# Kernel optimization log

Measured on AMD Instinct MI355X. Metric: run time of the kernel, lower is better.

## Reference

```python
import jax, jax.numpy as jnp
import numpy as np

EMBED = 768
HEADS = 12
HEAD_DIM = EMBED // HEADS
HIDDEN = int(EMBED * 4.0)
EPS = 1e-5


def setup_inputs() -> dict:
    key = jax.random.key(0)
    ks = jax.random.split(key, 12)
    s = 0.02
    return {
        "x": jax.random.normal(ks[0], (8, 1024, EMBED), dtype=jnp.float32),
        # norm1 / norm2 (LayerNorm affine params)
        "g1": jnp.ones((EMBED,), jnp.float32),
        "b1": jnp.zeros((EMBED,), jnp.float32),
        "g2": jnp.ones((EMBED,), jnp.float32),
        "b2": jnp.zeros((EMBED,), jnp.float32),
        # attention weights (stored [in, out]; qkv_bias=False)
        "w_qkv": jax.random.normal(ks[1], (EMBED, 3 * EMBED), jnp.float32) * s,
        "w_proj": jax.random.normal(ks[2], (EMBED, EMBED), jnp.float32) * s,
        "b_proj": jnp.zeros((EMBED,), jnp.float32),
        # MLP weights
        "w_fc1": jax.random.normal(ks[3], (EMBED, HIDDEN), jnp.float32) * s,
        "b_fc1": jnp.zeros((HIDDEN,), jnp.float32),
        "w_fc2": jax.random.normal(ks[4], (HIDDEN, EMBED), jnp.float32) * s,
        "b_fc2": jnp.zeros((EMBED,), jnp.float32),
    }


def _layernorm(x, g, b):
    mu = jnp.mean(x, axis=-1, keepdims=True)
    var = jnp.var(x, axis=-1, keepdims=True)
    return (x - mu) * jax.lax.rsqrt(var + EPS) * g + b


def reference(x, g1, b1, g2, b2, w_qkv, w_proj, b_proj, w_fc1, b_fc1, w_fc2, b_fc2):
    B, N, C = x.shape
    scaling = HEAD_DIM ** (-0.5)

    # --- attention branch ---
    h = _layernorm(x, g1, b1)
    qkv = (h @ w_qkv).reshape(B, N, 3, HEADS, HEAD_DIM)
    q, k, v = qkv[:, :, 0], qkv[:, :, 1], qkv[:, :, 2]  # [B, N, H, D]
    attn = jnp.einsum("bnhd,bmhd->bhnm", q, k) * scaling  # full NxN scores
    attn = jax.nn.softmax(attn, axis=-1)
    out = jnp.einsum("bhnm,bmhd->bnhd", attn, v).reshape(B, N, C)
    out = out @ w_proj + b_proj
    x = x + out

    # --- MLP branch ---
    h = _layernorm(x, g2, b2)
    h = jax.nn.gelu(h @ w_fc1 + b_fc1, approximate=False)
    h = h @ w_fc2 + b_fc2
    return x + h
```

## Files before the change

### kernel.cpp

```cpp
#include <hip/hip_runtime.h>
#include <hip/hip_bf16.h>
#include <math.h>

#define EMBED 768
#define HEADS 12
#define HEAD_DIM 64
#define HIDDEN 3072
#define SEQ 1024
#define BATCH 8
#define TOKENS (SEQ*BATCH)

typedef unsigned short u16;
typedef __attribute__((ext_vector_type(8))) short bf16x8;
typedef __attribute__((ext_vector_type(4))) float floatx4;
typedef __attribute__((ext_vector_type(4))) u16 u16x4;
typedef __attribute__((ext_vector_type(2))) u16 u16x2;

__device__ __forceinline__ u16 f2bf(float f){
    union { float f; unsigned u; } v; v.f = f;
    unsigned r = v.u + 0x7fffu + ((v.u >> 16) & 1u);
    return (u16)(r >> 16);
}

__device__ __forceinline__ void gload16(const void* g, void* l){
    __builtin_amdgcn_global_load_lds((const __attribute__((address_space(1))) void*)g,
                                     (__attribute__((address_space(3))) void*)l, 16, 0, 0);
}

__device__ __forceinline__ float gelu_fast(float x){
    float t = 1.5957691216f * (x + 0.044715f * x * x * x);
    return x / (1.0f + __expf(-t));
}

__global__ void transpose_cast_all(const float* __restrict__ w0, const float* __restrict__ w1,
                                   const float* __restrict__ w2, const float* __restrict__ w3,
                                   u16* __restrict__ o0, u16* __restrict__ o1,
                                   u16* __restrict__ o2, u16* __restrict__ o3){
    int bb = blockIdx.x;
    const float* W; u16* Wt; int K, N, bx, by;
    if(bb < 1728)      { int l = bb;        W=w0; Wt=o0; K=768;  N=2304; bx=l%72; by=l/72; }
    else if(bb < 2304) { int l = bb-1728;   W=w1; Wt=o1; K=768;  N=768;  bx=l%24; by=l/24; }
    else if(bb < 4608) { int l = bb-2304;   W=w2; Wt=o2; K=768;  N=3072; bx=l%96; by=l/96; }
    else               { int l = bb-4608;   W=w3; Wt=o3; K=3072; N=768;  bx=l%24; by=l/24; }

    __shared__ float tile[32][33];
    int n0 = bx * 32, k0 = by * 32;
    int tx = threadIdx.x, ty = threadIdx.y;
    #pragma unroll
    for(int i=0;i<32;i+=8) tile[ty+i][tx] = W[(size_t)(k0+ty+i)*N + n0+tx];
    __syncthreads();
    int tid = ty*32 + tx;
    int kp = (tid & 15)*2, nn = tid >> 4;
    #pragma unroll
    for(int p=0;p<2;p++){
        int n = nn + p*16;
        u16x2 w2v;
        w2v.x = f2bf(tile[kp  ][n]);
        w2v.y = f2bf(tile[kp+1][n]);
        *(u16x2*)(Wt + (size_t)(n0+n)*K + k0 + kp) = w2v;
    }
}

__global__ __launch_bounds__(256) void ln_kernel(const float* __restrict__ x, const float* __restrict__ g,
                                                 const float* __restrict__ b, u16* __restrict__ out){
    int row  = blockIdx.x * 4 + (threadIdx.x >> 6);
    int lane = threadIdx.x & 63;
    const float4* xr = (const float4*)(x + (size_t)row * EMBED);
    float4 v[3];
    float s = 0.f;
    #pragma unroll
    for(int i=0;i<3;i++){
        v[i] = xr[i*64 + lane];
        s += v[i].x + v[i].y + v[i].z + v[i].w;
    }
    #pragma unroll
    for(int o=32;o>0;o>>=1) s += __shfl_xor(s, o);
    float mu = s * (1.0f/EMBED);
    float s2 = 0.f;
    #pragma unroll
    for(int i=0;i<3;i++){
        float dx = v[i].x-mu, dy = v[i].y-mu, dz = v[i].z-mu, dw = v[i].w-mu;
        s2 += dx*dx + dy*dy + dz*dz + dw*dw;
    }
    #pragma unroll
    for(int o=32;o>0;o>>=1) s2 += __shfl_xor(s2, o);
    float rstd = rsqrtf(s2*(1.0f/EMBED) + 1e-5f);
    u16* orow = out + (size_t)row * EMBED;
    const float4* g4 = (const float4*)g;
    const float4* b4 = (const float4*)b;
    #pragma unroll
    for(int i=0;i<3;i++){
        int c4 = i*64 + lane;
        float4 gv = g4[c4], bv = b4[c4];
        u16x4 pk;
        pk.x = f2bf((v[i].x-mu)*rstd*gv.x + bv.x);
        pk.y = f2bf((v[i].y-mu)*rstd*gv.y + bv.y);
        pk.z = f2bf((v[i].z-mu)*rstd*gv.z + bv.z);
        pk.w = f2bf((v[i].w-mu)*rstd*gv.w + bv.w);
        *(u16x4*)(orow + c4*4) = pk;
    }
}

template<int EPI, int BM>
__global__ __launch_bounds__(256) void gemm_bt(const u16* __restrict__ A, const u16* __restrict__ Bt,
        void* __restrict__ Cout, const float* __restrict__ bias, const float* __restrict__ res,
        u16* __restrict__ vt, int M, int N, int K, int ldc){
    constexpr int MF  = BM/32;
    constexpr int ASZ = BM*64;
    constexpr int BSZ = 128*64;
    __shared__ __align__(16) u16 As[2*ASZ];
    __shared__ __align__(16) u16 Bs[2*BSZ];
    int tid  = threadIdx.x;
    int wave = tid >> 6, lane = tid & 63;
    int quad = lane >> 4, lm = lane & 15;
    int m0 = blockIdx.y * BM, n0 = blockIdx.x * 128;
    int wm = (wave & 1) * (BM/2);
    int wn = (wave >> 1) * 64;

    floatx4 acc[MF][4];
    #pragma unroll
    for(int i=0;i<MF;i++)
        #pragma unroll
        for(int j=0;j<4;j++) acc[i][j] = (floatx4){0.f,0.f,0.f,0.f};

    int srow = tid >> 3;
    int scol = ((tid & 7) ^ (srow & 7)) * 8;
    const u16* aP[MF];
    const u16* bP[4];
    #pragma unroll
    for(int p=0;p<MF;p++) aP[p] = A  + (size_t)(m0 + p*32 + srow) * K + scol;
    #pragma unroll
    for(int p=0;p<4;p++)  bP[p] = Bt + (size_t)(n0 + p*32 + srow) * K + scol;

    #pragma unroll
    for(int p=0;p<MF;p++) gload16(aP[p], As + p*2048 + tid*8);
    #pragma unroll
    for(int p=0;p<4;p++)  gload16(bP[p], Bs + p*2048 + tid*8);
    __syncthreads();

    int cur = 0;
    for(int k0=0; k0<K; k0+=64){
        int nxt = cur ^ 1;
        if(k0 + 64 < K){
            #pragma unroll
            for(int p=0;p<MF;p++) gload16(aP[p] + k0 + 64, As + nxt*ASZ + p*2048 + tid*8);
            #pragma unroll
            for(int p=0;p<4;p++)  gload16(bP[p] + k0 + 64, Bs + nxt*BSZ + p*2048 + tid*8);
        }
        const u16* Asb = As + cur*ASZ;
        const u16* Bsb = Bs + cur*BSZ;
        #pragma unroll
        for(int ks=0;ks<2;ks++){
            int slotoff = (((ks*4+quad) ^ (lm&7)) << 3);
            bf16x8 af[MF], bfr[4];
            #pragma unroll
            for(int i=0;i<MF;i++)
                af[i]  = *(const bf16x8*)(Asb + (wm + i*16 + lm)*64 + slotoff);
            #pragma unroll
            for(int i=0;i<4;i++)
                bfr[i] = *(const bf16x8*)(Bsb + (wn + i*16 + lm)*64 + slotoff);
            #pragma unroll
            for(int mf=0;mf<MF;mf++)
                #pragma unroll
                for(int nf=0;nf<4;nf++)
                    acc[mf][nf] = __builtin_amdgcn_mfma_f32_16x16x32_bf16(af[mf], bfr[nf], acc[mf][nf], 0, 0, 0);
        }
        if(k0 + 64 < K) __syncthreads();
        cur = nxt;
    }

    if(EPI == 3 && n0 >= 1536){
        #pragma unroll
        for(int nf=0;nf<4;nf++){
            int col = n0 + wn + nf*16 + lm;
            int hh = (col - 1536) >> 6;
            int d  = col & 63;
            #pragma unroll
            for(int mf=0;mf<MF;mf++){
                int row0 = m0 + wm + mf*16 + quad*4;
                int bb  = row0 >> 10;
                int key = row0 & 1023;
                u16x4 pk;
                #pragma unroll
                for(int r=0;r<4;r++) pk[r] = f2bf(acc[mf][nf][r]);
                *(u16x4*)(vt + ((size_t)(bb*HEADS+hh)*64 + d)*SEQ + key) = pk;
            }
        }
        return;
    }

    #pragma unroll
    for(int nf=0;nf<4;nf++){
        int col = n0 + wn + nf*16 + lm;
        float bv = bias ? bias[col] : 0.f;
        #pragma unroll
        for(int mf=0;mf<MF;mf++){
            int row0 = m0 + wm + mf*16 + quad*4;
            #pragma unroll
            for(int r=0;r<4;r++){
                float v = acc[mf][nf][r] + bv;
                size_t idx = (size_t)(row0 + r) * ldc + col;
                if(EPI == 1){
                    v = gelu_fast(v);
                    ((u16*)Cout)[idx] = f2bf(v);
                } else if(EPI == 2){
                    ((float*)Cout)[idx] = v + res[idx];
                } else {
                    ((u16*)Cout)[idx] = f2bf(v);
                }
            }
        }
    }
}

__global__ __launch_bounds__(256) void attn_kernel(const u16* __restrict__ qk, const u16* __restrict__ vt,
                                                   u16* __restrict__ out){
    int qt = blockIdx.x, h = blockIdx.y, b = blockIdx.z;
    int tid = threadIdx.x;
    int wave = tid >> 6, lane = tid & 63;
    int quad = lane >> 4, lm = lane & 15;

    __shared__ __align__(16) u16 Ks[2*64*64];
    __shared__ __align__(16) u16 Vs[2*64*64];
    __shared__ __align__(16) u16 P[4*32*64];

    const u16* qbase = qk + (size_t)b * SEQ * 1536;
    const u16* vbase = vt + (size_t)(b*HEADS + h) * 64 * SEQ;
    u16* Pw = P + wave*2048;

    int q0 = qt*128 + wave*32;
    bf16x8 qf[2][2];
    #pragma unroll
    for(int qi=0;qi<2;qi++){
        const u16* qp = qbase + (size_t)(q0 + qi*16 + lm)*1536 + h*64;
        qf[qi][0] = *(const bf16x8*)(qp + quad*8);
        qf[qi][1] = *(const bf16x8*)(qp + 32 + quad*8);
    }

    float l_i[2] = {0.f, 0.f};
    floatx4 o_acc[2][4];
    #pragma unroll
    for(int qi=0;qi<2;qi++)
        #pragma unroll
        for(int nf=0;nf<4;nf++) o_acc[qi][nf] = (floatx4){0.f,0.f,0.f,0.f};

    int sr = lane >> 3;
    int sp = lane & 7;
    const float C = 0.18033688011112186f;

    auto stage = [&](int kt, int buf){
        #pragma unroll
        for(int i=0;i<2;i++){
            int rr = wave*16 + i*8 + sr;
            int sw = (sp ^ (rr & 7)) * 8;
            gload16(qbase + (size_t)(kt*64 + rr)*1536 + 768 + h*64 + sw,
                    Ks + buf*4096 + (wave*16 + i*8)*64 + lane*8);
            gload16(vbase + (size_t)rr*SEQ + kt*64 + sw,
                    Vs + buf*4096 + (wave*16 + i*8)*64 + lane*8);
        }
    };

    stage(0, 0);
    __syncthreads();

    int cur = 0;
    for(int kt=0; kt<16; kt++){
        if(kt < 15) stage(kt+1, cur^1);
        const u16* Ksb = Ks + cur*4096;
        const u16* Vsb = Vs + cur*4096;

        floatx4 s[4][2];
        #pragma unroll
        for(int kf=0;kf<4;kf++){
            int krow = kf*16 + lm;
            bf16x8 k0 = *(const bf16x8*)(Ksb + krow*64 + ((quad     ^ (lm&7))*8));
            bf16x8 k1 = *(const bf16x8*)(Ksb + krow*64 + (((4+quad) ^ (lm&7))*8));
            #pragma unroll
            for(int qi=0;qi<2;qi++){
                floatx4 t = (floatx4){0.f,0.f,0.f,0.f};
                t = __builtin_amdgcn_mfma_f32_16x16x32_bf16(k0, qf[qi][0], t, 0, 0, 0);
                t = __builtin_amdgcn_mfma_f32_16x16x32_bf16(k1, qf[qi][1], t, 0, 0, 0);
                s[kf][qi] = t;
            }
        }

        #pragma unroll
        for(int qi=0;qi<2;qi++){
            float part = 0.f;
            #pragma unroll
            for(int kf=0;kf<4;kf++){
                #pragma unroll
                for(int r=0;r<4;r++){
                    float e = exp2f(s[kf][qi][r]*C);
                    s[kf][qi][r] = e;
                    part += e;
                }
            }
            part += __shfl_xor(part, 16);
            part += __shfl_xor(part, 32);
            l_i[qi] += part;
            #pragma unroll
            for(int kf=0;kf<4;kf++){
                u16x4 pk;
                #pragma unroll
                for(int r=0;r<4;r++) pk[r] = f2bf(s[kf][qi][r]);
                int c  = kf*4 + quad;
                int cp = c ^ (2*(lm & 7));
                *(u16x4*)(Pw + (qi*16 + lm)*64 + cp*4) = pk;
            }
        }

        #pragma unroll
        for(int ks=0;ks<2;ks++){
            bf16x8 vf[4];
            #pragma unroll
            for(int nf=0;nf<4;nf++)
                vf[nf] = *(const bf16x8*)(Vsb + (nf*16+lm)*64 + (((ks*4+quad) ^ (lm&7))*8));
            #pragma unroll
            for(int qi=0;qi<2;qi++){
                int cr = (ks*8 + 2*quad) ^ (2*(lm & 7));
                bf16x8 pa = *(const bf16x8*)(Pw + (qi*16 + lm)*64 + cr*4);
                #pragma unroll
                for(int nf=0;nf<4;nf++)
                    o_acc[qi][nf] = __builtin_amdgcn_mfma_f32_16x16x32_bf16(pa, vf[nf], o_acc[qi][nf], 0, 0, 0);
            }
        }
        if(kt < 15) __syncthreads();
        cur ^= 1;
    }

    #pragma unroll
    for(int qi=0;qi<2;qi++){
        float rl[4];
        #pragma unroll
        for(int r=0;r<4;r++) rl[r] = 1.0f / __shfl(l_i[qi], quad*4 + r);
        int token = b*SEQ + qt*128 + wave*32 + qi*16 + quad*4;
        #pragma unroll
        for(int nf=0;nf<4;nf++){
            #pragma unroll
            for(int r=0;r<4;r++){
                out[(size_t)(token + r)*EMBED + h*64 + nf*16 + lm] = f2bf(o_acc[qi][nf][r] * rl[r]);
            }
        }
    }
}

extern "C" void kernel_launch(void* const* d_in, const int* in_sizes, int n_in,
                              void* d_out, int out_size, void* d_ws, size_t ws_size,
                              hipStream_t stream) {
    const float* x      = (const float*)d_in[0];
    const float* g1     = (const float*)d_in[1];
    const float* b1     = (const float*)d_in[2];
    const float* g2     = (const float*)d_in[3];
    const float* b2     = (const float*)d_in[4];
    const float* w_qkv  = (const float*)d_in[5];
    const float* w_proj = (const float*)d_in[6];
    const float* b_proj = (const float*)d_in[7];
    const float* w_fc1  = (const float*)d_in[8];
    const float* b_fc1  = (const float*)d_in[9];
    const float* w_fc2  = (const float*)d_in[10];
    const float* b_fc2  = (const float*)d_in[11];
    float* out = (float*)d_out;

    char* ws = (char*)d_ws;
    u16*   wqkv_t  = (u16*)  (ws + 0);
    u16*   wproj_t = (u16*)  (ws + 3538944);
    u16*   wfc1_t  = (u16*)  (ws + 4718592);
    u16*   wfc2_t  = (u16*)  (ws + 9437184);
    float* x1      = (float*)(ws + 14155776);
    u16*   hbuf    = (u16*)  (ws + 39321600);
    u16*   qkbuf   = (u16*)  (ws + 51904512);
    u16*   vtbuf   = (u16*)  (ws + 77070336);
    u16*   attn_o  = (u16*)  (ws + 89653248);
    u16*   fc1_o   = qkbuf;
    u16*   h2      = hbuf;

    transpose_cast_all<<<6912, dim3(32,8), 0, stream>>>(w_qkv, w_proj, w_fc1, w_fc2,
                                                        wqkv_t, wproj_t, wfc1_t, wfc2_t);

    ln_kernel<<<TOKENS/4, 256, 0, stream>>>(x, g1, b1, hbuf);

    gemm_bt<3,128><<<dim3(2304/128, TOKENS/128), 256, 0, stream>>>(hbuf, wqkv_t, qkbuf, nullptr, nullptr, vtbuf, TOKENS, 2304, 768, 1536);

    attn_kernel<<<dim3(8, HEADS, BATCH), 256, 0, stream>>>(qkbuf, vtbuf, attn_o);

    gemm_bt<2,64><<<dim3( 768/128, TOKENS/64), 256, 0, stream>>>(attn_o, wproj_t, x1, b_proj, x, nullptr, TOKENS, 768, 768, 768);

    ln_kernel<<<TOKENS/4, 256, 0, stream>>>(x1, g2, b2, h2);

    gemm_bt<1,128><<<dim3(3072/128, TOKENS/128), 256, 0, stream>>>(h2, wfc1_t, fc1_o, b_fc1, nullptr, nullptr, TOKENS, 3072, 768, 3072);

    gemm_bt<2,64><<<dim3( 768/128, TOKENS/64), 256, 0, stream>>>(fc1_o, wfc2_t, out, b_fc2, x1, nullptr, TOKENS, 768, 3072, 768);
}
```

Measured before the change: 381.2 us.

## Replace GEMM with 256x256 tile, 8-wave kernel with interleaved prefetch and barriers

Replaces the 128-wide GEMM with a 256x256 tile kernel using 512 threads, where each wave computes a 128x64 sub-tile. Next-tile global loads are split across four phases interleaved with MFMA groups, with s_setprio raised around the MFMA bursts and explicit barriers between phases. Larger tiles raise data reuse per LDS load. The 768-wide GEMMs now launch only 96 blocks, which underfills the GPU, and the doubled LDS footprint limits occupancy.

After: 512.3 us. 1.34x slower.

```diff
diff --git a/kernel.cpp b/kernel.cpp
--- a/kernel.cpp
+++ b/kernel.cpp
@@ -101,72 +101,91 @@
     }
 }
 
-template<int EPI, int BM>
-__global__ __launch_bounds__(256) void gemm_bt(const u16* __restrict__ A, const u16* __restrict__ Bt,
+template<int EPI>
+__global__ __launch_bounds__(512,2) void gemm256(const u16* __restrict__ A, const u16* __restrict__ Bt,
         void* __restrict__ Cout, const float* __restrict__ bias, const float* __restrict__ res,
         u16* __restrict__ vt, int M, int N, int K, int ldc){
-    constexpr int MF  = BM/32;
-    constexpr int ASZ = BM*64;
-    constexpr int BSZ = 128*64;
-    __shared__ __align__(16) u16 As[2*ASZ];
-    __shared__ __align__(16) u16 Bs[2*BSZ];
+    __shared__ __align__(16) u16 As[2*16384];
+    __shared__ __align__(16) u16 Bs[2*16384];
     int tid  = threadIdx.x;
     int wave = tid >> 6, lane = tid & 63;
     int quad = lane >> 4, lm = lane & 15;
-    int m0 = blockIdx.y * BM, n0 = blockIdx.x * 128;
-    int wm = (wave & 1) * (BM/2);
-    int wn = (wave >> 1) * 64;
-
-    floatx4 acc[MF][4];
-    #pragma unroll
-    for(int i=0;i<MF;i++)
+    int wm = (wave >> 2) * 128;
+    int wn = (wave & 3) * 64;
+    int m0 = blockIdx.y * 256, n0 = blockIdx.x * 256;
+
+    floatx4 acc[8][4];
+    #pragma unroll
+    for(int i=0;i<8;i++)
         #pragma unroll
         for(int j=0;j<4;j++) acc[i][j] = (floatx4){0.f,0.f,0.f,0.f};
 
     int srow = tid >> 3;
     int scol = ((tid & 7) ^ (srow & 7)) * 8;
-    const u16* aP[MF];
-    const u16* bP[4];
-    #pragma unroll
-    for(int p=0;p<MF;p++) aP[p] = A  + (size_t)(m0 + p*32 + srow) * K + scol;
-    #pragma unroll
-    for(int p=0;p<4;p++)  bP[p] = Bt + (size_t)(n0 + p*32 + srow) * K + scol;
-
-    #pragma unroll
-    for(int p=0;p<MF;p++) gload16(aP[p], As + p*2048 + tid*8);
-    #pragma unroll
-    for(int p=0;p<4;p++)  gload16(bP[p], Bs + p*2048 + tid*8);
-    __syncthreads();
-
-    int cur = 0;
-    for(int k0=0; k0<K; k0+=64){
-        int nxt = cur ^ 1;
-        if(k0 + 64 < K){
-            #pragma unroll
-            for(int p=0;p<MF;p++) gload16(aP[p] + k0 + 64, As + nxt*ASZ + p*2048 + tid*8);
-            #pragma unroll
-            for(int p=0;p<4;p++)  gload16(bP[p] + k0 + 64, Bs + nxt*BSZ + p*2048 + tid*8);
-        }
-        const u16* Asb = As + cur*ASZ;
-        const u16* Bsb = Bs + cur*BSZ;
-        #pragma unroll
-        for(int ks=0;ks<2;ks++){
-            int slotoff = (((ks*4+quad) ^ (lm&7)) << 3);
-            bf16x8 af[MF], bfr[4];
-            #pragma unroll
-            for(int i=0;i<MF;i++)
-                af[i]  = *(const bf16x8*)(Asb + (wm + i*16 + lm)*64 + slotoff);
-            #pragma unroll
-            for(int i=0;i<4;i++)
-                bfr[i] = *(const bf16x8*)(Bsb + (wn + i*16 + lm)*64 + slotoff);
-            #pragma unroll
-            for(int mf=0;mf<MF;mf++)
+    const u16* aR[4];
+    const u16* bR[4];
+    #pragma unroll
+    for(int h=0;h<2;h++)
+        #pragma unroll
+        for(int i=0;i<2;i++){
+            aR[h*2+i] = A  + (size_t)(m0 + h*128 + i*64 + srow) * K + scol;
+            bR[h*2+i] = Bt + (size_t)(n0 + h*128 + i*64 + srow) * K + scol;
+        }
+
+    int nt = K / 64;
+
+    #pragma unroll
+    for(int p=0;p<4;p++) gload16(aR[p], As + p*4096 + tid*8);
+    #pragma unroll
+    for(int p=0;p<4;p++) gload16(bR[p], Bs + p*4096 + tid*8);
+    asm volatile("s_waitcnt vmcnt(0)" ::: "memory");
+    __builtin_amdgcn_s_barrier();
+
+    for(int t=0; t<nt; ++t){
+        int cur = t & 1, nxt = cur ^ 1;
+        size_t koff = (size_t)(t+1) * 64;
+        bool pf = (t+1 < nt);
+        const u16* Ac = As + cur*16384;
+        const u16* Bc = Bs + cur*16384;
+        bf16x8 bfr[4][2];
+        #pragma unroll
+        for(int q=0;q<4;q++){
+            if(pf){
+                if(q<2){
+                    gload16(aR[q*2  ] + koff, As + nxt*16384 + (q*2  )*4096 + tid*8);
+                    gload16(aR[q*2+1] + koff, As + nxt*16384 + (q*2+1)*4096 + tid*8);
+                } else {
+                    gload16(bR[(q-2)*2  ] + koff, Bs + nxt*16384 + ((q-2)*2  )*4096 + tid*8);
+                    gload16(bR[(q-2)*2+1] + koff, Bs + nxt*16384 + ((q-2)*2+1)*4096 + tid*8);
+                }
+            }
+            if(q==0){
                 #pragma unroll
                 for(int nf=0;nf<4;nf++)
-                    acc[mf][nf] = __builtin_amdgcn_mfma_f32_16x16x32_bf16(af[mf], bfr[nf], acc[mf][nf], 0, 0, 0);
-        }
-        if(k0 + 64 < K) __syncthreads();
-        cur = nxt;
+                    #pragma unroll
+                    for(int ks=0;ks<2;ks++)
+                        bfr[nf][ks] = *(const bf16x8*)(Bc + (wn + nf*16 + lm)*64 + (((ks*4+quad) ^ (lm&7))*8));
+            }
+            bf16x8 af[2][2];
+            #pragma unroll
+            for(int mf2=0;mf2<2;mf2++)
+                #pragma unroll
+                for(int ks=0;ks<2;ks++)
+                    af[mf2][ks] = *(const bf16x8*)(Ac + (wm + (q*2+mf2)*16 + lm)*64 + (((ks*4+quad) ^ (lm&7))*8));
+
+            __builtin_amdgcn_s_barrier();
+            __builtin_amdgcn_s_setprio(1);
+            #pragma unroll
+            for(int mf2=0;mf2<2;mf2++)
+                #pragma unroll
+                for(int nf=0;nf<4;nf++)
+                    #pragma unroll
+                    for(int ks=0;ks<2;ks++)
+                        acc[q*2+mf2][nf] = __builtin_amdgcn_mfma_f32_16x16x32_bf16(af[mf2][ks], bfr[nf][ks], acc[q*2+mf2][nf], 0, 0, 0);
+            __builtin_amdgcn_s_setprio(0);
+            if(q==3) asm volatile("s_waitcnt vmcnt(0)" ::: "memory");
+            __builtin_amdgcn_s_barrier();
+        }
     }
 
     if(EPI == 3 && n0 >= 1536){
@@ -176,7 +195,7 @@
             int hh = (col - 1536) >> 6;
             int d  = col & 63;
             #pragma unroll
-            for(int mf=0;mf<MF;mf++){
+            for(int mf=0;mf<8;mf++){
                 int row0 = m0 + wm + mf*16 + quad*4;
                 int bb  = row0 >> 10;
                 int key = row0 & 1023;
@@ -194,7 +213,7 @@
         int col = n0 + wn + nf*16 + lm;
         float bv = bias ? bias[col] : 0.f;
         #pragma unroll
-        for(int mf=0;mf<MF;mf++){
+        for(int mf=0;mf<8;mf++){
             int row0 = m0 + wm + mf*16 + quad*4;
             #pragma unroll
             for(int r=0;r<4;r++){
@@ -380,15 +399,15 @@
 
     ln_kernel<<<TOKENS/4, 256, 0, stream>>>(x, g1, b1, hbuf);
 
-    gemm_bt<3,128><<<dim3(2304/128, TOKENS/128), 256, 0, stream>>>(hbuf, wqkv_t, qkbuf, nullptr, nullptr, vtbuf, TOKENS, 2304, 768, 1536);
+    gemm256<3><<<dim3(2304/256, TOKENS/256), 512, 0, stream>>>(hbuf, wqkv_t, qkbuf, nullptr, nullptr, vtbuf, TOKENS, 2304, 768, 1536);
 
     attn_kernel<<<dim3(8, HEADS, BATCH), 256, 0, stream>>>(qkbuf, vtbuf, attn_o);
 
-    gemm_bt<2,64><<<dim3( 768/128, TOKENS/64), 256, 0, stream>>>(attn_o, wproj_t, x1, b_proj, x, nullptr, TOKENS, 768, 768, 768);
+    gemm256<2><<<dim3( 768/256, TOKENS/256), 512, 0, stream>>>(attn_o, wproj_t, x1, b_proj, x, nullptr, TOKENS, 768, 768, 768);
 
     ln_kernel<<<TOKENS/4, 256, 0, stream>>>(x1, g2, b2, h2);
 
-    gemm_bt<1,128><<<dim3(3072/128, TOKENS/128), 256, 0, stream>>>(h2, wfc1_t, fc1_o, b_fc1, nullptr, nullptr, TOKENS, 3072, 768, 3072);
-
-    gemm_bt<2,64><<<dim3( 768/128, TOKENS/64), 256, 0, stream>>>(fc1_o, wfc2_t, out, b_fc2, x1, nullptr, TOKENS, 768, 3072, 768);
-}
+    gemm256<1><<<dim3(3072/256, TOKENS/256), 512, 0, stream>>>(h2, wfc1_t, fc1_o, b_fc1, nullptr, nullptr, TOKENS, 3072, 768, 3072);
+
+    gemm256<2><<<dim3( 768/256, TOKENS/256), 512, 0, stream>>>(fc1_o, wfc2_t, out, b_fc2, x1, nullptr, TOKENS, 768, 3072, 768);
+}
```
